# Kernel tuning notes

Hardware: AMD Instinct MI355X
Metric: run time of the kernel (lower is better)

The kernel has to match this reference:

```python
import jax, jax.numpy as jnp
import numpy as np

# Dimensions / config (WorldModelConfig + PredictiveLayerConfig defaults)
S, N, L = 128, 256, 3          # n_sensory, n_hidden, n_layers
T, B = 100, 512                # timesteps, batch
TAU_MEM, TAU_PRED, DT = 20.0, 50.0, 1.0
NOISE_STD, ERROR_GAIN = 0.02, 0.5
DECAY_MEM = float(np.exp(-DT / TAU_MEM))
DECAY_PRED = float(np.exp(-DT / TAU_PRED))
ALPHA = DT / TAU_PRED          # precision EMA rate


def setup_inputs() -> dict:
    key = jax.random.key(0)
    ks = jax.random.split(key, 12)
    w = lambda k, a, b, s: jax.random.normal(k, (a, b), dtype=jnp.float32) * s
    return {
        'sensory_seq': jax.random.uniform(ks[0], (T, B, S), dtype=jnp.float32),
        'ff0': w(ks[1], S, N, 0.1 / S ** 0.5),
        'ff1': w(ks[2], N, N, 0.1 / N ** 0.5),
        'ff2': w(ks[3], N, N, 0.1 / N ** 0.5),
        'rec0': w(ks[4], N, N, 0.01),
        'rec1': w(ks[5], N, N, 0.01),
        'rec2': w(ks[6], N, N, 0.01),
        'pred0': w(ks[7], N, N, 0.1 / N ** 0.5),
        'pred1': w(ks[8], N, N, 0.1 / N ** 0.5),
        'p2r0': w(ks[9], N, N, 0.1 / N ** 0.5),
        'p2r1': w(ks[10], N, N, 0.1 / N ** 0.5),
    }


def _lif(v, inp, decay, noise):
    """LIF membrane update: leak + drive + noise, threshold=1.0, reset to 0."""
    v = decay * v + inp + noise
    s = (v >= 1.0).astype(v.dtype)
    return s, v * (1.0 - s)


def reference(sensory_seq, ff0, ff1, ff2, rec0, rec1, rec2, pred0, pred1, p2r0, p2r1):
    ffs = [ff0, ff1, ff2]
    recs = [rec0, rec1, rec2]
    preds = [pred0, pred1]
    p2rs = [p2r0, p2r1]
    mask = 1.0 - jnp.eye(N, dtype=sensory_seq.dtype)   # recurrent_mask
    base_key = jax.random.key(42)
    Bsz = sensory_seq.shape[1]

    init = (
        jnp.zeros((L, Bsz, N), jnp.float32),   # repr membrane
        jnp.zeros((2, Bsz, N), jnp.float32),   # pred membrane (layers 0,1)
        jnp.zeros((L, Bsz, N), jnp.float32),   # last spikes
        jnp.ones((L, Bsz, N), jnp.float32),    # precision
    )

    def step(carry, t):
        v, pv, last, prec = carry
        nks = jax.random.split(jax.random.fold_in(base_key, t), 5)
        new_v, new_pv, new_last, new_prec, errs = [], [], [], [], []
        for i in range(L):
            # top-down prediction from layer i+1's previous-step activity
            if i < L - 1:
                pred_in = last[i + 1] @ preds[i]
                pn = (NOISE_STD * 0.5) * jax.random.normal(nks[3 + i], (Bsz, N))
                psp, pvi = _lif(pv[i], pred_in, DECAY_PRED, pn)
                prediction = psp @ p2rs[i]
                new_pv.append(pvi)
            else:
                prediction = jnp.zeros((Bsz, N), jnp.float32)
            # bottom-up input: sensory for layer 0, lower layer's current spikes above
            inp_act = sensory_seq[t] if i == 0 else new_last[i - 1]
            input_repr = inp_act @ ffs[i]
            error = input_repr - prediction
            total = prediction + error * ERROR_GAIN * prec[i] + last[i] @ (recs[i] * mask)
            noi = NOISE_STD * jax.random.normal(nks[i], (Bsz, N))
            sp, vi = _lif(v[i], total, DECAY_MEM, noi)
            # precision EMA on inverse error variance
            ev = jnp.mean(error * error, axis=1, keepdims=True) + 1e-6
            pr = (1.0 - ALPHA) * prec[i] + ALPHA * (1.0 / ev)
            new_v.append(vi); new_last.append(sp); new_prec.append(pr); errs.append(error)
        carry = (jnp.stack(new_v), jnp.stack(new_pv), jnp.stack(new_last), jnp.stack(new_prec))
        return carry, jnp.stack(errs)   # [L, B, N] per step

    _, errors = jax.lax.scan(step, init, jnp.arange(T))
    return errors   # [T, L, B, N]
```

## Files before the change

kernel.cpp:

```cpp
#include <hip/hip_runtime.h>
#include <stdint.h>

#define TSTEPS 100
#define BATCH  512
#define NH     256
#define NS     128

__device__ __forceinline__ uint32_t rotl32(uint32_t x, int r) {
  return (x << r) | (x >> (32 - r));
}

__device__ __forceinline__ void tf2x32(uint32_t k0, uint32_t k1,
                                       uint32_t c0, uint32_t c1,
                                       uint32_t& o0, uint32_t& o1) {
  const uint32_t ks2 = k0 ^ k1 ^ 0x1BD11BDAu;
  uint32_t x0 = c0 + k0, x1 = c1 + k1;
#define TFR(r) { x0 += x1; x1 = rotl32(x1, r); x1 ^= x0; }
  TFR(13) TFR(15) TFR(26) TFR(6)
  x0 += k1;  x1 += ks2 + 1u;
  TFR(17) TFR(29) TFR(16) TFR(24)
  x0 += ks2; x1 += k0 + 2u;
  TFR(13) TFR(15) TFR(26) TFR(6)
  x0 += k0;  x1 += k1 + 3u;
  TFR(17) TFR(29) TFR(16) TFR(24)
  x0 += k1;  x1 += ks2 + 4u;
  TFR(13) TFR(15) TFR(26) TFR(6)
  x0 += ks2; x1 += k0 + 5u;
#undef TFR
  o0 = x0; o1 = x1;
}

__device__ __forceinline__ float xla_vf32_log(float a) {
  uint32_t bits = __float_as_uint(a);
  float e = __fadd_rn((float)((int)(bits >> 23) - 127), 1.0f);
  float x = __uint_as_float((bits & 0x007FFFFFu) | 0x3F000000u);
  const bool mask = x < 0.707106781186547524f;
  float tmp = mask ? x : 0.0f;
  x = __fsub_rn(x, 1.0f);
  e = mask ? __fsub_rn(e, 1.0f) : e;
  x = __fadd_rn(x, tmp);
  float z = __fmul_rn(x, x);
  float y = 7.0376836292e-2f;
  y = __fmaf_rn(y, x, -1.1514610310e-1f);
  y = __fmaf_rn(y, x, 1.1676998740e-1f);
  y = __fmaf_rn(y, x, -1.2420140846e-1f);
  y = __fmaf_rn(y, x, 1.4249322787e-1f);
  y = __fmaf_rn(y, x, -1.6668057665e-1f);
  y = __fmaf_rn(y, x, 2.0000714765e-1f);
  y = __fmaf_rn(y, x, -2.4999993993e-1f);
  y = __fmaf_rn(y, x, 3.3333331174e-1f);
  y = __fmul_rn(y, x);
  y = __fmul_rn(y, z);
  y = __fmaf_rn(e, -2.12194440e-4f, y);
  y = __fmaf_rn(-0.5f, z, y);
  x = __fadd_rn(x, y);
  x = __fmaf_rn(e, 0.693359375f, x);
  return x;
}

__device__ __forceinline__ float xla_sqrt2_erfinv(float u) {
  float nxx = -__fmul_rn(u, u);
  float w;
  if (fabsf(nxx) < 1e-4f) {
    w = -__fmul_rn(__fmaf_rn(-0.5f, nxx, 1.0f), nxx);
  } else {
    w = -xla_vf32_log(__fadd_rn(nxx, 1.0f));
  }
  float p;
  if (w < 5.0f) {
    float t = __fsub_rn(w, 2.5f);
    p = 2.81022636e-08f;
    p = __fmaf_rn(p, t, 3.43273939e-07f);
    p = __fmaf_rn(p, t, -3.5233877e-06f);
    p = __fmaf_rn(p, t, -4.39150654e-06f);
    p = __fmaf_rn(p, t, 0.00021858087f);
    p = __fmaf_rn(p, t, -0.00125372503f);
    p = __fmaf_rn(p, t, -0.00417768164f);
    p = __fmaf_rn(p, t, 0.246640727f);
    p = __fmaf_rn(p, t, 1.50140941f);
  } else {
    float t = __fsub_rn(__fsqrt_rn(w), 3.0f);
    p = -0.000200214257f;
    p = __fmaf_rn(p, t, 0.000100950558f);
    p = __fmaf_rn(p, t, 0.00134934322f);
    p = __fmaf_rn(p, t, -0.00367342844f);
    p = __fmaf_rn(p, t, 0.00573950773f);
    p = __fmaf_rn(p, t, -0.0076224613f);
    p = __fmaf_rn(p, t, 0.00943887047f);
    p = __fmaf_rn(p, t, 1.00167406f);
    p = __fmaf_rn(p, t, 2.83297682f);
  }
  return __fmul_rn((float)1.4142135623730951, __fmul_rn(p, u));
}

__device__ __forceinline__ float jax_normal(uint32_t k0, uint32_t k1, uint32_t j) {
  uint32_t o0, o1;
  tf2x32(k0, k1, 0u, j, o0, o1);
  const uint32_t bits = o0 ^ o1;
  float f = __fsub_rn(__uint_as_float((bits >> 9) | 0x3f800000u), 1.0f);
  const float LO = -0.99999994f;
  float u = __fmaf_rn(f, 2.0f, LO);
  u = fmaxf(LO, u);
  return xla_sqrt2_erfinv(u);
}

__global__ void pack_w(const float* __restrict__ src, float* __restrict__ dst,
                       int K, int zero_diag) {
  int tid = blockIdx.x * 256 + threadIdx.x;
  if (tid >= K * NH) return;
  int k = tid >> 8, n = tid & 255;
  float v = src[tid];
  if (zero_diag && k == n) v = 0.f;
  dst[(((k >> 2) * NH) + n) * 4 + (k & 3)] = v;
}

__global__ __launch_bounds__(256)
void gen_noise(float* __restrict__ NZ) {
  uint32_t idx = blockIdx.x * 256u + threadIdx.x;
  uint32_t j = idx & 131071u;
  uint32_t td = idx >> 17;
  uint32_t t = td / 5u, d = td - 5u * t;
  uint32_t fk0, fk1, k0, k1;
  tf2x32(0u, 42u, 0u, t, fk0, fk1);
  tf2x32(fk0, fk1, 0u, d, k0, k1);
  float z = jax_normal(k0, k1, j);
  float scale = (d >= 3u) ? 0.01f : 0.02f;
  NZ[idx] = __fmul_rn(scale, z);
}

__device__ __forceinline__ void dotW2r(const float4* __restrict__ P,
                                       const float* __restrict__ X0,
                                       const float* __restrict__ X1,
                                       int n, int k4b, int k4e,
                                       float& r0, float& r1) {
  float a0 = r0, a1 = r1;
  #pragma unroll 8
  for (int k4 = k4b; k4 < k4e; ++k4) {
    float4 w = P[k4 * NH + n];
    float4 x0 = *(const float4*)(X0 + 4 * k4);
    float4 x1 = *(const float4*)(X1 + 4 * k4);
    a0 = __fmaf_rn(x0.x, w.x, a0); a1 = __fmaf_rn(x1.x, w.x, a1);
    a0 = __fmaf_rn(x0.y, w.y, a0); a1 = __fmaf_rn(x1.y, w.y, a1);
    a0 = __fmaf_rn(x0.z, w.z, a0); a1 = __fmaf_rn(x1.z, w.z, a1);
    a0 = __fmaf_rn(x0.w, w.w, a0); a1 = __fmaf_rn(x1.w, w.w, a1);
  }
  r0 = a0; r1 = a1;
}

__device__ __forceinline__ void dot2W2r(const float4* __restrict__ PA,
                                        const float* __restrict__ XA0,
                                        const float* __restrict__ XA1,
                                        const float4* __restrict__ PB,
                                        const float* __restrict__ XB0,
                                        const float* __restrict__ XB1,
                                        int n, int k4b, int k4e,
                                        float& rA0, float& rA1,
                                        float& rB0, float& rB1) {
  float a0 = rA0, a1 = rA1, b0 = rB0, b1 = rB1;
  #pragma unroll 4
  for (int k4 = k4b; k4 < k4e; ++k4) {
    float4 wa = PA[k4 * NH + n];
    float4 wb = PB[k4 * NH + n];
    float4 xa0 = *(const float4*)(XA0 + 4 * k4);
    float4 xa1 = *(const float4*)(XA1 + 4 * k4);
    float4 xb0 = *(const float4*)(XB0 + 4 * k4);
    float4 xb1 = *(const float4*)(XB1 + 4 * k4);
    a0 = __fmaf_rn(xa0.x, wa.x, a0); a1 = __fmaf_rn(xa1.x, wa.x, a1);
    b0 = __fmaf_rn(xb0.x, wb.x, b0); b1 = __fmaf_rn(xb1.x, wb.x, b1);
    a0 = __fmaf_rn(xa0.y, wa.y, a0); a1 = __fmaf_rn(xa1.y, wa.y, a1);
    b0 = __fmaf_rn(xb0.y, wb.y, b0); b1 = __fmaf_rn(xb1.y, wb.y, b1);
    a0 = __fmaf_rn(xa0.z, wa.z, a0); a1 = __fmaf_rn(xa1.z, wa.z, a1);
    b0 = __fmaf_rn(xb0.z, wb.z, b0); b1 = __fmaf_rn(xb1.z, wb.z, b1);
    a0 = __fmaf_rn(xa0.w, wa.w, a0); a1 = __fmaf_rn(xa1.w, wa.w, a1);
    b0 = __fmaf_rn(xb0.w, wb.w, b0); b1 = __fmaf_rn(xb1.w, wb.w, b1);
  }
  rA0 = a0; rA1 = a1; rB0 = b0; rB1 = b1;
}

__global__ __launch_bounds__(512)
void wm_fast7(const float* __restrict__ sensory,
              const float4* __restrict__ pred0p, const float4* __restrict__ pred1p,
              const float4* __restrict__ p2r0p,  const float4* __restrict__ rec0p,
              const float4* __restrict__ ff0p,   const float4* __restrict__ p2r1p,
              const float4* __restrict__ ff1p,   const float4* __restrict__ rec1p,
              const float4* __restrict__ ff2p,   const float4* __restrict__ rec2p,
              const float* __restrict__ NZ,
              float* __restrict__ out) {
  const int tid = threadIdx.x;
  const int n = tid & 255;
  const int h = tid >> 8;
  const int b0 = blockIdx.x * 2, b1 = b0 + 1;

  __shared__ __align__(16) float last[2][3][2][NH];
  __shared__ __align__(16) float psp0[2][NH];
  __shared__ __align__(16) float psp1[2][NH];
  __shared__ __align__(16) float sens[2][NS];
  __shared__ __align__(16) float errsq[3][2][NH];
  __shared__ __align__(16) float xfer[2][NH];
  __shared__ float evsum[3][2];

  if (h == 0) {
    #pragma unroll
    for (int i = 0; i < 3; ++i) {
      last[0][i][0][n] = 0.f; last[0][i][1][n] = 0.f;
      last[1][i][0][n] = 0.f; last[1][i][1][n] = 0.f;
    }
  }

  float pvR0 = 0.f, pvR1 = 0.f;
  float vX0 = 0.f, vX1 = 0.f;
  float vY0 = 0.f, vY1 = 0.f;
  float p0a = 1.f, p0b = 1.f, p1a = 1.f, p1b = 1.f, p2a = 1.f, p2b = 1.f;
  const float DM = (float)0.951229424500714009;
  const float DP = (float)0.980198673306755250;

  __syncthreads();

  for (int t = 0; t < TSTEPS; ++t) {
    const int p = t & 1, q = p ^ 1;
    const size_t t5 = (size_t)t * 5 * BATCH * NH;
#define NZI(d, bb) (t5 + ((size_t)(d) * BATCH + (bb)) * NH + n)

    if (tid < 2 * NS) {
      int rr = tid >> 7, kk = tid & 127;
      sens[rr][kk] = sensory[((size_t)t * BATCH + b0 + rr) * NS + kk];
    }
    if (h == 0) {
      float a0 = 0.f, a1 = 0.f;
      dotW2r(pred0p, last[p][1][0], last[p][1][1], n, 0, 64, a0, a1);
      float pn0 = NZ[NZI(3, b0)], pn1 = NZ[NZI(3, b1)];
      pvR0 = __fadd_rn(__fmaf_rn(DP, pvR0, a0), pn0);
      bool s0 = (pvR0 >= 1.0f);
      psp0[0][n] = s0 ? 1.f : 0.f;
      pvR0 = s0 ? 0.f : pvR0;
      pvR1 = __fadd_rn(__fmaf_rn(DP, pvR1, a1), pn1);
      bool s1 = (pvR1 >= 1.0f);
      psp0[1][n] = s1 ? 1.f : 0.f;
      pvR1 = s1 ? 0.f : pvR1;
    } else {
      float a0 = 0.f, a1 = 0.f;
      dotW2r(pred1p, last[p][2][0], last[p][2][1], n, 0, 64, a0, a1);
      float pn0 = NZ[NZI(4, b0)], pn1 = NZ[NZI(4, b1)];
      pvR0 = __fadd_rn(__fmaf_rn(DP, pvR0, a0), pn0);
      bool s0 = (pvR0 >= 1.0f);
      psp1[0][n] = s0 ? 1.f : 0.f;
      pvR0 = s0 ? 0.f : pvR0;
      pvR1 = __fadd_rn(__fmaf_rn(DP, pvR1, a1), pn1);
      bool s1 = (pvR1 >= 1.0f);
      psp1[1][n] = s1 ? 1.f : 0.f;
      pvR1 = s1 ? 0.f : pvR1;
    }
    __syncthreads();

    float sA0 = 0.f, sA1 = 0.f, sB0 = 0.f, sB1 = 0.f;
    if (h == 0) {
      dot2W2r(ff0p, sens[0], sens[1], rec0p, last[p][0][0], last[p][0][1],
              n, 0, 32, sA0, sA1, sB0, sB1);
      dotW2r(rec0p, last[p][0][0], last[p][0][1], n, 32, 64, sB0, sB1);
    } else {
      float pr0 = 0.f, pr1 = 0.f;
      dotW2r(p2r0p, psp0[0], psp0[1], n, 0, 64, pr0, pr1);
      xfer[0][n] = pr0; xfer[1][n] = pr1;
    }
    __syncthreads();
    if (h == 0) {
      float pr0 = xfer[0][n], pr1 = xfer[1][n];
      float noi0 = NZ[NZI(0, b0)], noi1 = NZ[NZI(0, b1)];
      float e0 = __fsub_rn(sA0, pr0), e1 = __fsub_rn(sA1, pr1);
      out[(((size_t)t * 3 + 0) * BATCH + b0) * NH + n] = e0;
      out[(((size_t)t * 3 + 0) * BATCH + b1) * NH + n] = e1;
      errsq[0][0][n] = __fmul_rn(e0, e0);
      errsq[0][1][n] = __fmul_rn(e1, e1);
      float m0 = __fmul_rn(e0, 0.5f), m1 = __fmul_rn(e1, 0.5f);
      float t0 = __fadd_rn(__fmaf_rn(m0, p0a, pr0), sB0);
      float t1 = __fadd_rn(__fmaf_rn(m1, p0b, pr1), sB1);
      vX0 = __fadd_rn(__fmaf_rn(DM, vX0, t0), noi0);
      vX1 = __fadd_rn(__fmaf_rn(DM, vX1, t1), noi1);
      bool s0 = (vX0 >= 1.0f), s1 = (vX1 >= 1.0f);
      last[q][0][0][n] = s0 ? 1.f : 0.f;
      last[q][0][1][n] = s1 ? 1.f : 0.f;
      vX0 = s0 ? 0.f : vX0; vX1 = s1 ? 0.f : vX1;
    }
    __syncthreads();

    if (h == 0) {
      float i0 = 0.f, i1 = 0.f;
      dotW2r(ff1p, last[q][0][0], last[q][0][1], n, 0, 64, i0, i1);
      xfer[0][n] = i0; xfer[1][n] = i1;
    } else {
      dot2W2r(p2r1p, psp1[0], psp1[1], rec1p, last[p][1][0], last[p][1][1],
              n, 0, 64, sA0, sA1, sB0, sB1);
    }
    __syncthreads();
    if (h == 1) {
      float i0 = xfer[0][n], i1 = xfer[1][n];
      float noi0 = NZ[NZI(1, b0)], noi1 = NZ[NZI(1, b1)];
      float e0 = __fsub_rn(i0, sA0), e1 = __fsub_rn(i1, sA1);
      out[(((size_t)t * 3 + 1) * BATCH + b0) * NH + n] = e0;
      out[(((size_t)t * 3 + 1) * BATCH + b1) * NH + n] = e1;
      errsq[1][0][n] = __fmul_rn(e0, e0);
      errsq[1][1][n] = __fmul_rn(e1, e1);
      float m0 = __fmul_rn(e0, 0.5f), m1 = __fmul_rn(e1, 0.5f);
      float t0 = __fadd_rn(__fmaf_rn(m0, p1a, sA0), sB0);
      float t1 = __fadd_rn(__fmaf_rn(m1, p1b, sA1), sB1);
      vX0 = __fadd_rn(__fmaf_rn(DM, vX0, t0), noi0);
      vX1 = __fadd_rn(__fmaf_rn(DM, vX1, t1), noi1);
      bool s0 = (vX0 >= 1.0f), s1 = (vX1 >= 1.0f);
      last[q][1][0][n] = s0 ? 1.f : 0.f;
      last[q][1][1][n] = s1 ? 1.f : 0.f;
      vX0 = s0 ? 0.f : vX0; vX1 = s1 ? 0.f : vX1;
    }
    __syncthreads();

    if (h == 0) {
      sA0 = 0.f; sA1 = 0.f;
      dotW2r(ff2p, last[q][1][0], last[q][1][1], n, 0, 64, sA0, sA1);
    } else {
      float rc0 = 0.f, rc1 = 0.f;
      dotW2r(rec2p, last[p][2][0], last[p][2][1], n, 0, 64, rc0, rc1);
      xfer[0][n] = rc0; xfer[1][n] = rc1;
    }
    __syncthreads();
    if (h == 0) {
      float rc0 = xfer[0][n], rc1 = xfer[1][n];
      float noi0 = NZ[NZI(2, b0)], noi1 = NZ[NZI(2, b1)];
      float e0 = sA0, e1 = sA1;
      out[(((size_t)t * 3 + 2) * BATCH + b0) * NH + n] = e0;
      out[(((size_t)t * 3 + 2) * BATCH + b1) * NH + n] = e1;
      errsq[2][0][n] = __fmul_rn(e0, e0);
      errsq[2][1][n] = __fmul_rn(e1, e1);
      float m0 = __fmul_rn(e0, 0.5f), m1 = __fmul_rn(e1, 0.5f);
      float t0 = __fadd_rn(__fmaf_rn(m0, p2a, 0.0f), rc0);
      float t1 = __fadd_rn(__fmaf_rn(m1, p2b, 0.0f), rc1);
      vY0 = __fadd_rn(__fmaf_rn(DM, vY0, t0), noi0);
      vY1 = __fadd_rn(__fmaf_rn(DM, vY1, t1), noi1);
      bool s0 = (vY0 >= 1.0f), s1 = (vY1 >= 1.0f);
      last[q][2][0][n] = s0 ? 1.f : 0.f;
      last[q][2][1][n] = s1 ? 1.f : 0.f;
      vY0 = s0 ? 0.f : vY0; vY1 = s1 ? 0.f : vY1;
    }
    __syncthreads();

    if (tid < 6) {
      const int l = tid >> 1, rr = tid & 1;
      const float4* s4 = (const float4*)errsq[l][rr];
      float acc = 0.f;
      #pragma unroll 16
      for (int k4 = 0; k4 < 64; ++k4) {
        float4 v = s4[k4];
        acc = __fadd_rn(acc, v.x); acc = __fadd_rn(acc, v.y);
        acc = __fadd_rn(acc, v.z); acc = __fadd_rn(acc, v.w);
      }
      evsum[l][rr] = acc;
    }
    __syncthreads();

    {
      float ev;
      ev = __fadd_rn(__fmul_rn(evsum[0][0], 0.00390625f), 1e-6f);
      p0a = __fmaf_rn(0.98f, p0a, __fmul_rn(0.02f, 1.0f / ev));
      ev = __fadd_rn(__fmul_rn(evsum[0][1], 0.00390625f), 1e-6f);
      p0b = __fmaf_rn(0.98f, p0b, __fmul_rn(0.02f, 1.0f / ev));
      ev = __fadd_rn(__fmul_rn(evsum[1][0], 0.00390625f), 1e-6f);
      p1a = __fmaf_rn(0.98f, p1a, __fmul_rn(0.02f, 1.0f / ev));
      ev = __fadd_rn(__fmul_rn(evsum[1][1], 0.00390625f), 1e-6f);
      p1b = __fmaf_rn(0.98f, p1b, __fmul_rn(0.02f, 1.0f / ev));
      ev = __fadd_rn(__fmul_rn(evsum[2][0], 0.00390625f), 1e-6f);
      p2a = __fmaf_rn(0.98f, p2a, __fmul_rn(0.02f, 1.0f / ev));
      ev = __fadd_rn(__fmul_rn(evsum[2][1], 0.00390625f), 1e-6f);
      p2b = __fmaf_rn(0.98f, p2b, __fmul_rn(0.02f, 1.0f / ev));
    }
#undef NZI
  }
}

__device__ __forceinline__ float dot_lds(const float* __restrict__ a,
                                         const float* __restrict__ W,
                                         int n, int K) {
  float acc = 0.f;
  #pragma unroll 8
  for (int k = 0; k < K; ++k)
    acc = __fmaf_rn(a[k], W[k * NH + n], acc);
  return acc;
}

__device__ __forceinline__ float dot_rec(const float* __restrict__ a,
                                         const float* __restrict__ W, int n) {
  float acc = 0.f;
  #pragma unroll 8
  for (int k = 0; k < NH; ++k) {
    float w = (k == n) ? 0.f : W[k * NH + n];
    acc = __fmaf_rn(a[k], w, acc);
  }
  return acc;
}

__global__ __launch_bounds__(NH)
void wm_kernel_mono(const float* __restrict__ sensory,
                    const float* __restrict__ ff0, const float* __restrict__ ff1,
                    const float* __restrict__ ff2,
                    const float* __restrict__ rec0, const float* __restrict__ rec1,
                    const float* __restrict__ rec2,
                    const float* __restrict__ pred0, const float* __restrict__ pred1,
                    const float* __restrict__ p2r0, const float* __restrict__ p2r1,
                    float* __restrict__ out) {
  const int b = blockIdx.x;
  const int n = threadIdx.x;

  __shared__ float last[2][3][NH];
  __shared__ float psp[NH];
  __shared__ float sens[NS];
  __shared__ float errsq[3][NH];
  __shared__ float evsum[3];
  __shared__ uint32_t keys[TSTEPS][5][2];

  if (n < TSTEPS) {
    uint32_t fk0, fk1;
    tf2x32(0u, 42u, 0u, (uint32_t)n, fk0, fk1);
    #pragma unroll
    for (int i = 0; i < 5; ++i) {
      uint32_t s0, s1;
      tf2x32(fk0, fk1, 0u, (uint32_t)i, s0, s1);
      keys[n][i][0] = s0; keys[n][i][1] = s1;
    }
  }
  for (int i = 0; i < 3; ++i) { last[0][i][n] = 0.f; last[1][i][n] = 0.f; }

  float v0 = 0.f, v1 = 0.f, v2 = 0.f, pv0 = 0.f, pv1 = 0.f;
  float prec0 = 1.f, prec1 = 1.f, prec2 = 1.f;
  const float DM = (float)0.951229424500714009;
  const float DP = (float)0.980198673306755250;
  const uint32_t j = (uint32_t)(b * NH + n);

  __syncthreads();

  for (int t = 0; t < TSTEPS; ++t) {
    const int p = t & 1, q = p ^ 1;

    if (n < NS) sens[n] = sensory[((size_t)t * BATCH + b) * NS + n];
    {
      float acc = dot_lds(last[p][1], pred0, n, NH);
      float pn = __fmul_rn(0.01f, jax_normal(keys[t][3][0], keys[t][3][1], j));
      pv0 = __fadd_rn(__fmaf_rn(DP, pv0, acc), pn);
      bool s = (pv0 >= 1.0f);
      psp[n] = s ? 1.f : 0.f;
      pv0 = s ? 0.f : pv0;
    }
    __syncthreads();

    {
      float pr  = dot_lds(psp, p2r0, n, NH);
      float inp = dot_lds(sens, ff0, n, NS);
      float rc  = dot_rec(last[p][0], rec0, n);
      float err = __fsub_rn(inp, pr);
      out[(((size_t)t * 3 + 0) * BATCH + b) * NH + n] = err;
      errsq[0][n] = __fmul_rn(err, err);
      float m1  = __fmul_rn(err, 0.5f);
      float tot = __fadd_rn(__fmaf_rn(m1, prec0, pr), rc);
      float noi = __fmul_rn(0.02f, jax_normal(keys[t][0][0], keys[t][0][1], j));
      v0 = __fadd_rn(__fmaf_rn(DM, v0, tot), noi);
      bool s = (v0 >= 1.0f);
      last[q][0][n] = s ? 1.f : 0.f;
      v0 = s ? 0.f : v0;
    }
    __syncthreads();

    {
      float acc = dot_lds(last[p][2], pred1, n, NH);
      float pn = __fmul_rn(0.01f, jax_normal(keys[t][4][0], keys[t][4][1], j));
      pv1 = __fadd_rn(__fmaf_rn(DP, pv1, acc), pn);
      bool s = (pv1 >= 1.0f);
      psp[n] = s ? 1.f : 0.f;
      pv1 = s ? 0.f : pv1;
    }
    __syncthreads();

    {
      float pr  = dot_lds(psp, p2r1, n, NH);
      float inp = dot_lds(last[q][0], ff1, n, NH);
      float rc  = dot_rec(last[p][1], rec1, n);
      float err = __fsub_rn(inp, pr);
      out[(((size_t)t * 3 + 1) * BATCH + b) * NH + n] = err;
      errsq[1][n] = __fmul_rn(err, err);
      float m1  = __fmul_rn(err, 0.5f);
      float tot = __fadd_rn(__fmaf_rn(m1, prec1, pr), rc);
      float noi = __fmul_rn(0.02f, jax_normal(keys[t][1][0], keys[t][1][1], j));
      v1 = __fadd_rn(__fmaf_rn(DM, v1, tot), noi);
      bool s = (v1 >= 1.0f);
      last[q][1][n] = s ? 1.f : 0.f;
      v1 = s ? 0.f : v1;
    }
    __syncthreads();

    {
      float inp = dot_lds(last[q][1], ff2, n, NH);
      float rc  = dot_rec(last[p][2], rec2, n);
      float err = inp;
      out[(((size_t)t * 3 + 2) * BATCH + b) * NH + n] = err;
      errsq[2][n] = __fmul_rn(err, err);
      float m1  = __fmul_rn(err, 0.5f);
      float tot = __fadd_rn(__fmaf_rn(m1, prec2, 0.0f), rc);
      float noi = __fmul_rn(0.02f, jax_normal(keys[t][2][0], keys[t][2][1], j));
      v2 = __fadd_rn(__fmaf_rn(DM, v2, tot), noi);
      bool s = (v2 >= 1.0f);
      last[q][2][n] = s ? 1.f : 0.f;
      v2 = s ? 0.f : v2;
    }
    __syncthreads();

    if (((n & 63) == 0) && n < 192) {
      const float* s = errsq[n >> 6];
      float acc = 0.f;
      #pragma unroll 32
      for (int k = 0; k < NH; ++k) acc = __fadd_rn(acc, s[k]);
      evsum[n >> 6] = acc;
    }
    __syncthreads();

    {
      float ev0 = __fadd_rn(__fmul_rn(evsum[0], 0.00390625f), 1e-6f);
      float ev1 = __fadd_rn(__fmul_rn(evsum[1], 0.00390625f), 1e-6f);
      float ev2 = __fadd_rn(__fmul_rn(evsum[2], 0.00390625f), 1e-6f);
      prec0 = __fmaf_rn(0.98f, prec0, __fmul_rn(0.02f, 1.0f / ev0));
      prec1 = __fmaf_rn(0.98f, prec1, __fmul_rn(0.02f, 1.0f / ev1));
      prec2 = __fmaf_rn(0.98f, prec2, __fmul_rn(0.02f, 1.0f / ev2));
    }
  }
}

extern "C" void kernel_launch(void* const* d_in, const int* in_sizes, int n_in,
                              void* d_out, int out_size, void* d_ws, size_t ws_size,
                              hipStream_t stream) {
  (void)in_sizes; (void)n_in; (void)out_size;
  const float* sensory = (const float*)d_in[0];
  const float* ff0  = (const float*)d_in[1];
  const float* ff1  = (const float*)d_in[2];
  const float* ff2  = (const float*)d_in[3];
  const float* rec0 = (const float*)d_in[4];
  const float* rec1 = (const float*)d_in[5];
  const float* rec2 = (const float*)d_in[6];
  const float* pred0 = (const float*)d_in[7];
  const float* pred1 = (const float*)d_in[8];
  const float* p2r0 = (const float*)d_in[9];
  const float* p2r1 = (const float*)d_in[10];
  float* out = (float*)d_out;

  const size_t OFF_PRED0 = 0, OFF_PRED1 = 65536, OFF_P2R0 = 131072,
               OFF_REC0 = 196608, OFF_FF0 = 262144, OFF_P2R1 = 294912,
               OFF_FF1 = 360448, OFF_REC1 = 425984, OFF_FF2 = 491520,
               OFF_REC2 = 557056, OFF_NZ = 655360;
  const size_t NZ_FLOATS = (size_t)TSTEPS * 5 * BATCH * NH;
  const size_t NEED = (OFF_NZ + NZ_FLOATS) * sizeof(float);

  if (ws_size >= NEED) {
    float* W = (float*)d_ws;
    pack_w<<<dim3(NH * NH / 256), dim3(256), 0, stream>>>(pred0, W + OFF_PRED0, NH, 0);
    pack_w<<<dim3(NH * NH / 256), dim3(256), 0, stream>>>(pred1, W + OFF_PRED1, NH, 0);
    pack_w<<<dim3(NH * NH / 256), dim3(256), 0, stream>>>(p2r0,  W + OFF_P2R0,  NH, 0);
    pack_w<<<dim3(NH * NH / 256), dim3(256), 0, stream>>>(rec0,  W + OFF_REC0,  NH, 1);
    pack_w<<<dim3(NS * NH / 256), dim3(256), 0, stream>>>(ff0,   W + OFF_FF0,   NS, 0);
    pack_w<<<dim3(NH * NH / 256), dim3(256), 0, stream>>>(p2r1,  W + OFF_P2R1,  NH, 0);
    pack_w<<<dim3(NH * NH / 256), dim3(256), 0, stream>>>(ff1,   W + OFF_FF1,   NH, 0);
    pack_w<<<dim3(NH * NH / 256), dim3(256), 0, stream>>>(rec1,  W + OFF_REC1,  NH, 1);
    pack_w<<<dim3(NH * NH / 256), dim3(256), 0, stream>>>(ff2,   W + OFF_FF2,   NH, 0);
    pack_w<<<dim3(NH * NH / 256), dim3(256), 0, stream>>>(rec2,  W + OFF_REC2,  NH, 1);
    gen_noise<<<dim3((unsigned)(NZ_FLOATS / 256)), dim3(256), 0, stream>>>(W + OFF_NZ);
    wm_fast7<<<dim3(BATCH / 2), dim3(512), 0, stream>>>(
        sensory,
        (const float4*)(W + OFF_PRED0), (const float4*)(W + OFF_PRED1),
        (const float4*)(W + OFF_P2R0),  (const float4*)(W + OFF_REC0),
        (const float4*)(W + OFF_FF0),   (const float4*)(W + OFF_P2R1),
        (const float4*)(W + OFF_FF1),   (const float4*)(W + OFF_REC1),
        (const float4*)(W + OFF_FF2),   (const float4*)(W + OFF_REC2),
        W + OFF_NZ, out);
  } else {
    wm_kernel_mono<<<dim3(BATCH), dim3(NH), 0, stream>>>(
        sensory, ff0, ff1, ff2, rec0, rec1, rec2,
        pred0, pred1, p2r0, p2r1, out);
  }
}
```

Before: 4.525 ms.

## Store spike vectors as wave ballot bitmasks in scalar registers

Binary spike activity is no longer kept as float arrays in shared memory. Each wave now writes it as 64-bit ballot masks, which are read back with readfirstlane into scalar registers, and the matvecs select weights by bit tests instead of loading float4 activations from LDS. This is meant to remove most LDS traffic and bank pressure in the inner dot-product loops. In exchange there is bit-extraction and select overhead per FMA, which may raise VALU work and register use.

```diff
diff --git a/kernel.cpp b/kernel.cpp
--- a/kernel.cpp
+++ b/kernel.cpp
@@ -128,57 +128,125 @@
   NZ[idx] = __fmul_rn(scale, z);
 }
 
-__device__ __forceinline__ void dotW2r(const float4* __restrict__ P,
-                                       const float* __restrict__ X0,
-                                       const float* __restrict__ X1,
-                                       int n, int k4b, int k4e,
-                                       float& r0, float& r1) {
+__device__ __forceinline__ void read_mask(const uint64_t* __restrict__ s,
+                                          uint64_t m[4]) {
+  #pragma unroll
+  for (int i = 0; i < 4; ++i) {
+    uint2 v = *reinterpret_cast<const uint2*>(s + i);
+    uint32_t lo = (uint32_t)__builtin_amdgcn_readfirstlane((int)v.x);
+    uint32_t hi = (uint32_t)__builtin_amdgcn_readfirstlane((int)v.y);
+    m[i] = (((uint64_t)hi) << 32) | (uint64_t)lo;
+  }
+}
+
+#define XB(bits, bit) (((bits) & (bit)) ? 1.0f : 0.0f)
+
+__device__ __forceinline__ void dotM2r(const float4* __restrict__ P,
+                                       const uint64_t M0[4], const uint64_t M1[4],
+                                       int n, float& r0, float& r1) {
   float a0 = r0, a1 = r1;
-  #pragma unroll 8
-  for (int k4 = k4b; k4 < k4e; ++k4) {
-    float4 w = P[k4 * NH + n];
-    float4 x0 = *(const float4*)(X0 + 4 * k4);
-    float4 x1 = *(const float4*)(X1 + 4 * k4);
-    a0 = __fmaf_rn(x0.x, w.x, a0); a1 = __fmaf_rn(x1.x, w.x, a1);
-    a0 = __fmaf_rn(x0.y, w.y, a0); a1 = __fmaf_rn(x1.y, w.y, a1);
-    a0 = __fmaf_rn(x0.z, w.z, a0); a1 = __fmaf_rn(x1.z, w.z, a1);
-    a0 = __fmaf_rn(x0.w, w.w, a0); a1 = __fmaf_rn(x1.w, w.w, a1);
+  #pragma unroll
+  for (int i = 0; i < 4; ++i) {
+    const uint64_t m0 = M0[i], m1 = M1[i];
+    #pragma unroll 4
+    for (int kk = 0; kk < 16; ++kk) {
+      const int k4 = i * 16 + kk;
+      float4 w = P[k4 * NH + n];
+      uint32_t b0 = (uint32_t)(m0 >> (kk * 4)) & 0xFu;
+      uint32_t b1 = (uint32_t)(m1 >> (kk * 4)) & 0xFu;
+      a0 = __fmaf_rn(XB(b0, 1u), w.x, a0); a1 = __fmaf_rn(XB(b1, 1u), w.x, a1);
+      a0 = __fmaf_rn(XB(b0, 2u), w.y, a0); a1 = __fmaf_rn(XB(b1, 2u), w.y, a1);
+      a0 = __fmaf_rn(XB(b0, 4u), w.z, a0); a1 = __fmaf_rn(XB(b1, 4u), w.z, a1);
+      a0 = __fmaf_rn(XB(b0, 8u), w.w, a0); a1 = __fmaf_rn(XB(b1, 8u), w.w, a1);
+    }
   }
   r0 = a0; r1 = a1;
 }
 
-__device__ __forceinline__ void dot2W2r(const float4* __restrict__ PA,
-                                        const float* __restrict__ XA0,
-                                        const float* __restrict__ XA1,
+__device__ __forceinline__ void dot2M2r(const float4* __restrict__ PA,
+                                        const uint64_t A0[4], const uint64_t A1[4],
                                         const float4* __restrict__ PB,
-                                        const float* __restrict__ XB0,
-                                        const float* __restrict__ XB1,
-                                        int n, int k4b, int k4e,
+                                        const uint64_t B0[4], const uint64_t B1[4],
+                                        int n,
                                         float& rA0, float& rA1,
                                         float& rB0, float& rB1) {
   float a0 = rA0, a1 = rA1, b0 = rB0, b1 = rB1;
-  #pragma unroll 4
-  for (int k4 = k4b; k4 < k4e; ++k4) {
-    float4 wa = PA[k4 * NH + n];
-    float4 wb = PB[k4 * NH + n];
-    float4 xa0 = *(const float4*)(XA0 + 4 * k4);
-    float4 xa1 = *(const float4*)(XA1 + 4 * k4);
-    float4 xb0 = *(const float4*)(XB0 + 4 * k4);
-    float4 xb1 = *(const float4*)(XB1 + 4 * k4);
-    a0 = __fmaf_rn(xa0.x, wa.x, a0); a1 = __fmaf_rn(xa1.x, wa.x, a1);
-    b0 = __fmaf_rn(xb0.x, wb.x, b0); b1 = __fmaf_rn(xb1.x, wb.x, b1);
-    a0 = __fmaf_rn(xa0.y, wa.y, a0); a1 = __fmaf_rn(xa1.y, wa.y, a1);
-    b0 = __fmaf_rn(xb0.y, wb.y, b0); b1 = __fmaf_rn(xb1.y, wb.y, b1);
-    a0 = __fmaf_rn(xa0.z, wa.z, a0); a1 = __fmaf_rn(xa1.z, wa.z, a1);
-    b0 = __fmaf_rn(xb0.z, wb.z, b0); b1 = __fmaf_rn(xb1.z, wb.z, b1);
-    a0 = __fmaf_rn(xa0.w, wa.w, a0); a1 = __fmaf_rn(xa1.w, wa.w, a1);
-    b0 = __fmaf_rn(xb0.w, wb.w, b0); b1 = __fmaf_rn(xb1.w, wb.w, b1);
+  #pragma unroll
+  for (int i = 0; i < 4; ++i) {
+    const uint64_t ma0 = A0[i], ma1 = A1[i], mb0 = B0[i], mb1 = B1[i];
+    #pragma unroll 2
+    for (int kk = 0; kk < 16; ++kk) {
+      const int k4 = i * 16 + kk;
+      float4 wa = PA[k4 * NH + n];
+      float4 wb = PB[k4 * NH + n];
+      uint32_t qa0 = (uint32_t)(ma0 >> (kk * 4)) & 0xFu;
+      uint32_t qa1 = (uint32_t)(ma1 >> (kk * 4)) & 0xFu;
+      uint32_t qb0 = (uint32_t)(mb0 >> (kk * 4)) & 0xFu;
+      uint32_t qb1 = (uint32_t)(mb1 >> (kk * 4)) & 0xFu;
+      a0 = __fmaf_rn(XB(qa0, 1u), wa.x, a0); a1 = __fmaf_rn(XB(qa1, 1u), wa.x, a1);
+      b0 = __fmaf_rn(XB(qb0, 1u), wb.x, b0); b1 = __fmaf_rn(XB(qb1, 1u), wb.x, b1);
+      a0 = __fmaf_rn(XB(qa0, 2u), wa.y, a0); a1 = __fmaf_rn(XB(qa1, 2u), wa.y, a1);
+      b0 = __fmaf_rn(XB(qb0, 2u), wb.y, b0); b1 = __fmaf_rn(XB(qb1, 2u), wb.y, b1);
+      a0 = __fmaf_rn(XB(qa0, 4u), wa.z, a0); a1 = __fmaf_rn(XB(qa1, 4u), wa.z, a1);
+      b0 = __fmaf_rn(XB(qb0, 4u), wb.z, b0); b1 = __fmaf_rn(XB(qb1, 4u), wb.z, b1);
+      a0 = __fmaf_rn(XB(qa0, 8u), wa.w, a0); a1 = __fmaf_rn(XB(qa1, 8u), wa.w, a1);
+      b0 = __fmaf_rn(XB(qb0, 8u), wb.w, b0); b1 = __fmaf_rn(XB(qb1, 8u), wb.w, b1);
+    }
   }
   rA0 = a0; rA1 = a1; rB0 = b0; rB1 = b1;
 }
 
+__device__ __forceinline__ void dotFM2r(const float4* __restrict__ Pf,
+                                        const float* __restrict__ Xs0,
+                                        const float* __restrict__ Xs1,
+                                        const float4* __restrict__ Pm,
+                                        const uint64_t M0[4], const uint64_t M1[4],
+                                        int n,
+                                        float& rf0, float& rf1,
+                                        float& rm0, float& rm1) {
+  float f0 = rf0, f1 = rf1, g0 = rm0, g1 = rm1;
+  #pragma unroll
+  for (int i = 0; i < 2; ++i) {
+    const uint64_t m0 = M0[i], m1 = M1[i];
+    #pragma unroll 2
+    for (int kk = 0; kk < 16; ++kk) {
+      const int k4 = i * 16 + kk;
+      float4 wf = Pf[k4 * NH + n];
+      float4 wm = Pm[k4 * NH + n];
+      float4 x0 = *reinterpret_cast<const float4*>(Xs0 + 4 * k4);
+      float4 x1 = *reinterpret_cast<const float4*>(Xs1 + 4 * k4);
+      uint32_t b0 = (uint32_t)(m0 >> (kk * 4)) & 0xFu;
+      uint32_t b1 = (uint32_t)(m1 >> (kk * 4)) & 0xFu;
+      f0 = __fmaf_rn(x0.x, wf.x, f0); f1 = __fmaf_rn(x1.x, wf.x, f1);
+      g0 = __fmaf_rn(XB(b0, 1u), wm.x, g0); g1 = __fmaf_rn(XB(b1, 1u), wm.x, g1);
+      f0 = __fmaf_rn(x0.y, wf.y, f0); f1 = __fmaf_rn(x1.y, wf.y, f1);
+      g0 = __fmaf_rn(XB(b0, 2u), wm.y, g0); g1 = __fmaf_rn(XB(b1, 2u), wm.y, g1);
+      f0 = __fmaf_rn(x0.z, wf.z, f0); f1 = __fmaf_rn(x1.z, wf.z, f1);
+      g0 = __fmaf_rn(XB(b0, 4u), wm.z, g0); g1 = __fmaf_rn(XB(b1, 4u), wm.z, g1);
+      f0 = __fmaf_rn(x0.w, wf.w, f0); f1 = __fmaf_rn(x1.w, wf.w, f1);
+      g0 = __fmaf_rn(XB(b0, 8u), wm.w, g0); g1 = __fmaf_rn(XB(b1, 8u), wm.w, g1);
+    }
+  }
+  #pragma unroll
+  for (int i = 2; i < 4; ++i) {
+    const uint64_t m0 = M0[i], m1 = M1[i];
+    #pragma unroll 4
+    for (int kk = 0; kk < 16; ++kk) {
+      const int k4 = i * 16 + kk;
+      float4 wm = Pm[k4 * NH + n];
+      uint32_t b0 = (uint32_t)(m0 >> (kk * 4)) & 0xFu;
+      uint32_t b1 = (uint32_t)(m1 >> (kk * 4)) & 0xFu;
+      g0 = __fmaf_rn(XB(b0, 1u), wm.x, g0); g1 = __fmaf_rn(XB(b1, 1u), wm.x, g1);
+      g0 = __fmaf_rn(XB(b0, 2u), wm.y, g0); g1 = __fmaf_rn(XB(b1, 2u), wm.y, g1);
+      g0 = __fmaf_rn(XB(b0, 4u), wm.z, g0); g1 = __fmaf_rn(XB(b1, 4u), wm.z, g1);
+      g0 = __fmaf_rn(XB(b0, 8u), wm.w, g0); g1 = __fmaf_rn(XB(b1, 8u), wm.w, g1);
+    }
+  }
+  rf0 = f0; rf1 = f1; rm0 = g0; rm1 = g1;
+}
+
 __global__ __launch_bounds__(512)
-void wm_fast7(const float* __restrict__ sensory,
+void wm_fast8(const float* __restrict__ sensory,
               const float4* __restrict__ pred0p, const float4* __restrict__ pred1p,
               const float4* __restrict__ p2r0p,  const float4* __restrict__ rec0p,
               const float4* __restrict__ ff0p,   const float4* __restrict__ p2r1p,
@@ -189,23 +257,19 @@
   const int tid = threadIdx.x;
   const int n = tid & 255;
   const int h = tid >> 8;
+  const int lane = tid & 63;
+  const int wv = (tid & 255) >> 6;
   const int b0 = blockIdx.x * 2, b1 = b0 + 1;
 
-  __shared__ __align__(16) float last[2][3][2][NH];
-  __shared__ __align__(16) float psp0[2][NH];
-  __shared__ __align__(16) float psp1[2][NH];
+  __shared__ uint64_t lmask[2][3][2][4];
+  __shared__ uint64_t pmask0[2][4];
+  __shared__ uint64_t pmask1[2][4];
   __shared__ __align__(16) float sens[2][NS];
   __shared__ __align__(16) float errsq[3][2][NH];
   __shared__ __align__(16) float xfer[2][NH];
   __shared__ float evsum[3][2];
 
-  if (h == 0) {
-    #pragma unroll
-    for (int i = 0; i < 3; ++i) {
-      last[0][i][0][n] = 0.f; last[0][i][1][n] = 0.f;
-      last[1][i][0][n] = 0.f; last[1][i][1][n] = 0.f;
-    }
-  }
+  if (tid < 48) ((uint64_t*)lmask)[tid] = 0ull;
 
   float pvR0 = 0.f, pvR1 = 0.f;
   float vX0 = 0.f, vX1 = 0.f;
@@ -226,40 +290,50 @@
       sens[rr][kk] = sensory[((size_t)t * BATCH + b0 + rr) * NS + kk];
     }
     if (h == 0) {
+      uint64_t M0[4], M1[4];
+      read_mask(lmask[p][1][0], M0);
+      read_mask(lmask[p][1][1], M1);
       float a0 = 0.f, a1 = 0.f;
-      dotW2r(pred0p, last[p][1][0], last[p][1][1], n, 0, 64, a0, a1);
+      dotM2r(pred0p, M0, M1, n, a0, a1);
       float pn0 = NZ[NZI(3, b0)], pn1 = NZ[NZI(3, b1)];
       pvR0 = __fadd_rn(__fmaf_rn(DP, pvR0, a0), pn0);
       bool s0 = (pvR0 >= 1.0f);
-      psp0[0][n] = s0 ? 1.f : 0.f;
       pvR0 = s0 ? 0.f : pvR0;
       pvR1 = __fadd_rn(__fmaf_rn(DP, pvR1, a1), pn1);
       bool s1 = (pvR1 >= 1.0f);
-      psp0[1][n] = s1 ? 1.f : 0.f;
       pvR1 = s1 ? 0.f : pvR1;
+      uint64_t bm0 = __ballot(s0), bm1 = __ballot(s1);
+      if (lane == 0) { pmask0[0][wv] = bm0; pmask0[1][wv] = bm1; }
     } else {
+      uint64_t M0[4], M1[4];
+      read_mask(lmask[p][2][0], M0);
+      read_mask(lmask[p][2][1], M1);
       float a0 = 0.f, a1 = 0.f;
-      dotW2r(pred1p, last[p][2][0], last[p][2][1], n, 0, 64, a0, a1);
+      dotM2r(pred1p, M0, M1, n, a0, a1);
       float pn0 = NZ[NZI(4, b0)], pn1 = NZ[NZI(4, b1)];
       pvR0 = __fadd_rn(__fmaf_rn(DP, pvR0, a0), pn0);
       bool s0 = (pvR0 >= 1.0f);
-      psp1[0][n] = s0 ? 1.f : 0.f;
       pvR0 = s0 ? 0.f : pvR0;
       pvR1 = __fadd_rn(__fmaf_rn(DP, pvR1, a1), pn1);
       bool s1 = (pvR1 >= 1.0f);
-      psp1[1][n] = s1 ? 1.f : 0.f;
       pvR1 = s1 ? 0.f : pvR1;
+      uint64_t bm0 = __ballot(s0), bm1 = __ballot(s1);
+      if (lane == 0) { pmask1[0][wv] = bm0; pmask1[1][wv] = bm1; }
     }
     __syncthreads();
 
     float sA0 = 0.f, sA1 = 0.f, sB0 = 0.f, sB1 = 0.f;
     if (h == 0) {
-      dot2W2r(ff0p, sens[0], sens[1], rec0p, last[p][0][0], last[p][0][1],
-              n, 0, 32, sA0, sA1, sB0, sB1);
-      dotW2r(rec0p, last[p][0][0], last[p][0][1], n, 32, 64, sB0, sB1);
+      uint64_t M0[4], M1[4];
+      read_mask(lmask[p][0][0], M0);
+      read_mask(lmask[p][0][1], M1);
+      dotFM2r(ff0p, sens[0], sens[1], rec0p, M0, M1, n, sA0, sA1, sB0, sB1);
     } else {
+      uint64_t M0[4], M1[4];
+      read_mask(pmask0[0], M0);
+      read_mask(pmask0[1], M1);
       float pr0 = 0.f, pr1 = 0.f;
-      dotW2r(p2r0p, psp0[0], psp0[1], n, 0, 64, pr0, pr1);
+      dotM2r(p2r0p, M0, M1, n, pr0, pr1);
       xfer[0][n] = pr0; xfer[1][n] = pr1;
     }
     __syncthreads();
@@ -277,19 +351,26 @@
       vX0 = __fadd_rn(__fmaf_rn(DM, vX0, t0), noi0);
       vX1 = __fadd_rn(__fmaf_rn(DM, vX1, t1), noi1);
       bool s0 = (vX0 >= 1.0f), s1 = (vX1 >= 1.0f);
-      last[q][0][0][n] = s0 ? 1.f : 0.f;
-      last[q][0][1][n] = s1 ? 1.f : 0.f;
       vX0 = s0 ? 0.f : vX0; vX1 = s1 ? 0.f : vX1;
+      uint64_t bm0 = __ballot(s0), bm1 = __ballot(s1);
+      if (lane == 0) { lmask[q][0][0][wv] = bm0; lmask[q][0][1][wv] = bm1; }
     }
     __syncthreads();
 
     if (h == 0) {
+      uint64_t M0[4], M1[4];
+      read_mask(lmask[q][0][0], M0);
+      read_mask(lmask[q][0][1], M1);
       float i0 = 0.f, i1 = 0.f;
-      dotW2r(ff1p, last[q][0][0], last[q][0][1], n, 0, 64, i0, i1);
+      dotM2r(ff1p, M0, M1, n, i0, i1);
       xfer[0][n] = i0; xfer[1][n] = i1;
     } else {
-      dot2W2r(p2r1p, psp1[0], psp1[1], rec1p, last[p][1][0], last[p][1][1],
-              n, 0, 64, sA0, sA1, sB0, sB1);
+      uint64_t A0[4], A1[4], B0[4], B1[4];
+      read_mask(pmask1[0], A0);
+      read_mask(pmask1[1], A1);
+      read_mask(lmask[p][1][0], B0);
+      read_mask(lmask[p][1][1], B1);
+      dot2M2r(p2r1p, A0, A1, rec1p, B0, B1, n, sA0, sA1, sB0, sB1);
     }
     __syncthreads();
     if (h == 1) {
@@ -306,18 +387,24 @@
       vX0 = __fadd_rn(__fmaf_rn(DM, vX0, t0), noi0);
       vX1 = __fadd_rn(__fmaf_rn(DM, vX1, t1), noi1);
       bool s0 = (vX0 >= 1.0f), s1 = (vX1 >= 1.0f);
-      last[q][1][0][n] = s0 ? 1.f : 0.f;
-      last[q][1][1][n] = s1 ? 1.f : 0.f;
       vX0 = s0 ? 0.f : vX0; vX1 = s1 ? 0.f : vX1;
+      uint64_t bm0 = __ballot(s0), bm1 = __ballot(s1);
+      if (lane == 0) { lmask[q][1][0][wv] = bm0; lmask[q][1][1][wv] = bm1; }
     }
     __syncthreads();
 
     if (h == 0) {
+      uint64_t M0[4], M1[4];
+      read_mask(lmask[q][1][0], M0);
+      read_mask(lmask[q][1][1], M1);
       sA0 = 0.f; sA1 = 0.f;
-      dotW2r(ff2p, last[q][1][0], last[q][1][1], n, 0, 64, sA0, sA1);
+      dotM2r(ff2p, M0, M1, n, sA0, sA1);
     } else {
+      uint64_t M0[4], M1[4];
+      read_mask(lmask[p][2][0], M0);
+      read_mask(lmask[p][2][1], M1);
       float rc0 = 0.f, rc1 = 0.f;
-      dotW2r(rec2p, last[p][2][0], last[p][2][1], n, 0, 64, rc0, rc1);
+      dotM2r(rec2p, M0, M1, n, rc0, rc1);
       xfer[0][n] = rc0; xfer[1][n] = rc1;
     }
     __syncthreads();
@@ -335,9 +422,9 @@
       vY0 = __fadd_rn(__fmaf_rn(DM, vY0, t0), noi0);
       vY1 = __fadd_rn(__fmaf_rn(DM, vY1, t1), noi1);
       bool s0 = (vY0 >= 1.0f), s1 = (vY1 >= 1.0f);
-      last[q][2][0][n] = s0 ? 1.f : 0.f;
-      last[q][2][1][n] = s1 ? 1.f : 0.f;
       vY0 = s0 ? 0.f : vY0; vY1 = s1 ? 0.f : vY1;
+      uint64_t bm0 = __ballot(s0), bm1 = __ballot(s1);
+      if (lane == 0) { lmask[q][2][0][wv] = bm0; lmask[q][2][1][wv] = bm1; }
     }
     __syncthreads();
 
@@ -565,7 +652,7 @@
     pack_w<<<dim3(NH * NH / 256), dim3(256), 0, stream>>>(ff2,   W + OFF_FF2,   NH, 0);
     pack_w<<<dim3(NH * NH / 256), dim3(256), 0, stream>>>(rec2,  W + OFF_REC2,  NH, 1);
     gen_noise<<<dim3((unsigned)(NZ_FLOATS / 256)), dim3(256), 0, stream>>>(W + OFF_NZ);
-    wm_fast7<<<dim3(BATCH / 2), dim3(512), 0, stream>>>(
+    wm_fast8<<<dim3(BATCH / 2), dim3(512), 0, stream>>>(
         sensory,
         (const float4*)(W + OFF_PRED0), (const float4*)(W + OFF_PRED1),
         (const float4*)(W + OFF_P2R0),  (const float4*)(W + OFF_REC0),
```

Measured after the change: 4.324 ms, median of 2. 4.4% less time.
